# Kernel tuning notes

Hardware: AMD Instinct MI355X
Metric: run time of the kernel (lower is better)

Reference implementation:

```python
import jax, jax.numpy as jnp
import numpy as np

TOPK, NUM_CLASSES = 13, 80
ALPHA, BETA, GAMMA, EPS = 1.0, 5.0, 3.0, 1e-09


def _make_boxes(key, shape, img=640.0, wmin=10.0, wmax=120.0):
    k1, k2 = jax.random.split(key)
    cxy = jax.random.uniform(k1, shape[:-1] + (2,), minval=0.0, maxval=img)
    wh = jax.random.uniform(k2, shape[:-1] + (2,), minval=wmin, maxval=wmax)
    return jnp.concatenate([cxy - wh / 2, cxy + wh / 2], axis=-1)


def setup_inputs() -> dict:
    key = jax.random.key(0)
    ks = jax.random.split(key, 7)
    bs, A, C, n = 16, 8400, 80, 60
    return {
        'pd_scores': jax.random.uniform(ks[0], (bs, A, C), dtype=jnp.float32),
        'pd_bboxes': _make_boxes(ks[1], (bs, A, 4)),
        'pd_angles': jax.random.uniform(ks[2], (bs, A, 1), minval=0.0, maxval=90.0),
        'anc_points': jax.random.uniform(ks[3], (A, 2), minval=0.0, maxval=640.0),
        'gt_labels': jax.random.randint(ks[4], (bs, n, 1), 0, C, dtype=jnp.int32),
        'gt_bboxes': _make_boxes(ks[5], (bs, n, 4)),
        'gt_angles': jax.random.uniform(ks[6], (bs, n, 1), minval=0.0, maxval=90.0),
        'mask_gt': jnp.ones((bs, n, 1), jnp.float32),
        'epoch_num': 1,
    }


def _cos_fn(x, ar, beta=2.0):
    return 0.5 + 0.5 * jnp.cos(beta / ar * x / 180.0 * jnp.pi + jnp.pi * (1.0 - beta / (2.0 * ar)))


def _angle_measure(pd_angles, gt_angles, gt_bboxes):
    # gt area ratio w/h -> (bs, n, 1, 1)
    w = gt_bboxes[..., 2:3] - gt_bboxes[..., 0:1]
    h = gt_bboxes[..., 3:4] - gt_bboxes[..., 1:2]
    ar = (w / (h + 1e-05))[:, :, None, :]
    theta = jnp.abs(gt_angles[:, :, None, :] - pd_angles[:, None, :, :])  # (bs,n,A,1)
    av = 1.0 / ar / (2.0 - 1.0 / ar)
    mx = _cos_fn(0.0, ar)
    mn = _cos_fn(90.0, ar)
    r = (_cos_fn(theta, ar) - mn) / (mx - mn) * (1.0 - av) + av
    r = jnp.where(jnp.isnan(r), 0.0, r)
    return jnp.squeeze(r, -1)  # (bs, n, A)


def _pairwise_iou(gt, pd):
    # gt (bs,n,4), pd (bs,A,4) -> (bs,n,A)
    lt = jnp.maximum(gt[:, :, None, :2], pd[:, None, :, :2])
    rb = jnp.minimum(gt[:, :, None, 2:], pd[:, None, :, 2:])
    inter = jnp.clip(rb - lt, 0.0).prod(-1)
    a1 = jnp.clip(gt[..., 2:] - gt[..., :2], 0.0).prod(-1)[:, :, None]
    a2 = jnp.clip(pd[..., 2:] - pd[..., :2], 0.0).prod(-1)[:, None, :]
    return inter / (a1 + a2 - inter + EPS)


def _select_topk(metrics, topk_mask):
    bs, n, A = metrics.shape
    _, idxs = jax.lax.top_k(metrics, TOPK)
    idxs = jnp.where(topk_mask, idxs, 0)
    flat = idxs.reshape(bs * n, TOPK)
    cnt = jnp.zeros((bs * n, A), jnp.int32).at[jnp.arange(bs * n)[:, None], flat].add(1)
    cnt = cnt.reshape(bs, n, A)
    return jnp.where(cnt > 1, 0, cnt).astype(metrics.dtype)


def _select_highest_overlaps(mask_pos, overlaps, n):
    fg = mask_pos.sum(-2)                                   # (bs, A)
    multi = fg[:, None, :] > 1                              # (bs, 1, A)
    is_max = jax.nn.one_hot(overlaps.argmax(1), n, axis=1, dtype=mask_pos.dtype)  # (bs,n,A)
    mask_pos = jnp.where(multi, is_max, mask_pos)
    fg = mask_pos.sum(-2)
    tgt_idx = mask_pos.argmax(-2)                           # (bs, A)
    return tgt_idx, fg, mask_pos


def reference(pd_scores, pd_bboxes, pd_angles, anc_points, gt_labels, gt_bboxes, gt_angles, mask_gt, epoch_num):
    bs, A, C = pd_scores.shape
    n = gt_bboxes.shape[1]
    lab = gt_labels[..., 0].astype(jnp.int32)               # (bs, n)

    # bbox_scores: pd_scores[b, :, gt_label] -> (bs, n, A)
    pts = jnp.transpose(pd_scores, (0, 2, 1))               # (bs, C, A)
    bbox_scores = jnp.take_along_axis(pts, lab[:, :, None], axis=1)

    overlaps = _pairwise_iou(gt_bboxes, pd_bboxes)          # (bs, n, A)
    ang = _angle_measure(pd_angles, gt_angles, gt_bboxes)   # (bs, n, A)
    align = bbox_scores ** ALPHA * overlaps ** BETA * ang ** GAMMA

    # anchors-inside-gt mask (bs, n, A)
    lt = anc_points[None, None, :, :] - gt_bboxes[:, :, None, :2]
    rb = gt_bboxes[:, :, None, 2:] - anc_points[None, None, :, :]
    in_gts = (jnp.concatenate([lt, rb], -1).min(-1) > EPS).astype(align.dtype)

    topk_mask = jnp.broadcast_to(mask_gt > 0, (bs, n, TOPK))
    mask_topk = _select_topk(align * in_gts, topk_mask)
    mask_pos = mask_topk * in_gts * mask_gt                 # (bs, n, A)

    tgt_idx, fg, mask_pos = _select_highest_overlaps(mask_pos, overlaps, n)

    # gather per-anchor targets from flattened gt tensors
    off = tgt_idx + jnp.arange(bs, dtype=tgt_idx.dtype)[:, None] * n   # (bs, A)
    tlab = lab.reshape(-1)[off]
    tlab = jnp.where(tlab < 0, 0, tlab)
    tbb = gt_bboxes.reshape(-1, 4)[off]                     # (bs, A, 4)
    tang = gt_angles.reshape(-1, 1)[off]                    # (bs, A, 1)
    ts = jax.nn.one_hot(tlab, C, dtype=pd_scores.dtype)     # (bs, A, C)
    ts = jnp.where(fg[:, :, None] > 0, ts, 0.0)

    # normalized alignment metric scaling
    align = align * mask_pos
    pam = align.max(-1, keepdims=True)                      # (bs, n, 1)
    pov = (overlaps * mask_pos).max(-1, keepdims=True)      # (bs, n, 1)
    norm = (align * pov / (pam + EPS)).max(-2)[:, :, None]  # (bs, A, 1)
    ts = ts * norm

    return tlab, tbb, tang, ts, fg > 0
```

## Files before the change

kernel.cpp:

```cpp
#include <hip/hip_runtime.h>
#include <math.h>

#define TOPK 13
#define PI_F 3.14159265358979323846f
#define K1_WAVES 4

typedef unsigned int u32;
typedef unsigned long long u64;

__device__ __forceinline__ u32 ford(float f) {
    u32 u = __float_as_uint(f);
    return (u & 0x80000000u) ? ~u : (u | 0x80000000u);
}
__device__ __forceinline__ float funord(u32 o) {
    u32 u = (o & 0x80000000u) ? (o & 0x7FFFFFFFu) : ~o;
    return __uint_as_float(u);
}

__device__ __forceinline__ float iou_fn(float4 g, float4 p) {
    float ltx = fmaxf(g.x, p.x), lty = fmaxf(g.y, p.y);
    float rbx = fminf(g.z, p.z), rby = fminf(g.w, p.w);
    float inter = fmaxf(rbx - ltx, 0.0f) * fmaxf(rby - lty, 0.0f);
    float a1 = fmaxf(g.z - g.x, 0.0f) * fmaxf(g.w - g.y, 0.0f);
    float a2 = fmaxf(p.z - p.x, 0.0f) * fmaxf(p.w - p.y, 0.0f);
    return inter / (((a1 + a2) - inter) + 1e-9f);
}

struct RowParams { float av, bar, offc, mx, mn; };

__device__ __forceinline__ RowParams row_params(float4 g) {
    float w = g.z - g.x, h = g.w - g.y;
    float ar = w / (h + 1e-5f);
    float ia = 1.0f / ar;
    RowParams rp;
    rp.av = ia / (2.0f - ia);
    rp.bar = 2.0f / ar;
    rp.offc = PI_F * (1.0f - 2.0f / (2.0f * ar));
    rp.mx = 0.5f + 0.5f * cosf(rp.offc);
    rp.mn = 0.5f + 0.5f * cosf(rp.bar * 90.0f / 180.0f * PI_F + rp.offc);
    return rp;
}

__device__ __forceinline__ float ang_measure(const RowParams& rp, float theta) {
    float cfv = 0.5f + 0.5f * cosf(rp.bar * theta / 180.0f * PI_F + rp.offc);
    float r = (cfv - rp.mn) / (rp.mx - rp.mn) * (1.0f - rp.av) + rp.av;
    return isnan(r) ? 0.0f : r;
}

__device__ __forceinline__ float align_fn(float s, float iou, float r) {
    float iou2 = iou * iou;
    float iou5 = (iou2 * iou2) * iou;
    float r3 = (r * r) * r;
    return (s * iou5) * r3;
}

__device__ __forceinline__ void insert13(u64* arr, u64 key) {
    if (key > arr[TOPK - 1]) {
#pragma unroll
        for (int jj = 0; jj < TOPK; jj++) {
            u64 hi = arr[jj] > key ? arr[jj] : key;
            u64 lo = arr[jj] > key ? key : arr[jj];
            arr[jj] = hi;
            key = lo;
        }
    }
}

__global__ void k0_init(int* cnt, int* assign1, u32* pam, u32* pov, int BA, int BN) {
    int t = blockIdx.x * blockDim.x + threadIdx.x;
    if (t < BA) { cnt[t] = 0; assign1[t] = -1; }
    if (t < BN) { pam[t] = 0x80000000u; pov[t] = 0x80000000u; }
}

__global__ __launch_bounds__(256)
void k1_topk(const float* __restrict__ scores, const float* __restrict__ pbox,
             const float* __restrict__ pang, const float* __restrict__ anc,
             const int* __restrict__ glab, const float* __restrict__ gbox,
             const float* __restrict__ gang, const float* __restrict__ mgt,
             int* __restrict__ cnt, int* __restrict__ assign1,
             float* __restrict__ out,
             int bs, int A, int n, int C) {
    int j = blockIdx.x;
    int b = j % bs;
    int i = j / bs;
    int bi = b * n + i;
    int tid = threadIdx.x;
    int BA = bs * A;

    int nF4 = BA * (C / 4);
    int zCH = (nF4 + gridDim.x - 1) / gridDim.x;
    int zBeg = j * zCH + tid;
    int zEnd = min(j * zCH + zCH, nF4);
    float4* tsf4 = (float4*)(out + (size_t)BA * 6);
    const float4 z4 = make_float4(0.0f, 0.0f, 0.0f, 0.0f);

    float mg = mgt[bi];
    if (!(mg > 0.0f)) {
        for (; zBeg < zEnd; zBeg += 256) tsf4[zBeg] = z4;
        return;
    }

    float4 g = ((const float4*)gbox)[bi];
    int lab = glab[bi];
    float ga = gang[bi];
    RowParams rp = row_params(g);

    const float4* pb = ((const float4*)pbox) + (size_t)b * A;
    const float* pa = pang + (size_t)b * A;
    const float2* ac = (const float2*)anc;
    const float* sc = scores + (size_t)b * A * C + lab;

    u64 arr[TOPK];
#pragma unroll
    for (int jj = 0; jj < TOPK; jj++) arr[jj] = 0ull;
    u64 zkey = 0ull;

    int a = tid;
    float4 p = pb[a];
    float pav = pa[a];
    float2 apt = ac[a];
    float mnv = fminf(fminf(apt.x - g.x, apt.y - g.y), fminf(g.z - apt.x, g.w - apt.y));

    int nit = (A + 255) >> 8;
    int clampA = A - 1;
    for (int it = 0; it < nit; ++it) {
        int an = a + 256;
        int can = min(an, clampA);
        float4 p2 = pb[can];
        float pav2 = pa[can];
        float2 apt2 = ac[can];
        if (zBeg < zEnd) { tsf4[zBeg] = z4; zBeg += 256; }
        float mnv2 = fminf(fminf(apt2.x - g.x, apt2.y - g.y),
                           fminf(g.z - apt2.x, g.w - apt2.y));

        bool valid = a < A;
        float iou = iou_fn(g, p);
        bool needAlign = (mnv > 1e-9f) && (iou > 0.0f) && valid;
        if (needAlign || (zkey == 0ull && valid)) {
            float th = fabsf(ga - pav);
            float r = ang_measure(rp, th);
            bool zeroCand;
            if (needAlign && r > 0.0f) {
                float s = sc[(size_t)a * C];
                float v = align_fn(s, iou, r);
                if (v > 0.0f) {
                    zeroCand = false;
                    insert13(arr, ((u64)ford(v) << 32) | (u64)(0xFFFFFFFFu - (u32)a));
                } else {
                    zeroCand = true;
                }
            } else {
                zeroCand = (r >= 0.0f);
            }
            if (zeroCand && zkey == 0ull) {
                zkey = (0x80000000ull << 32) | (u64)(0xFFFFFFFFu - (u32)a);
            }
        }
        a = an; p = p2; pav = pav2; mnv = mnv2;
    }
    for (; zBeg < zEnd; zBeg += 256) tsf4[zBeg] = z4;
    insert13(arr, zkey);

    __shared__ u64 wtop[K1_WAVES * TOPK];
    int lane = tid & 63, wv = tid >> 6;
    for (int round = 0; round < TOPK; round++) {
        u64 m = arr[0];
#pragma unroll
        for (int st = 32; st > 0; st >>= 1) {
            u64 o = __shfl_xor(m, st, 64);
            if (o > m) m = o;
        }
        if (lane == 0) wtop[wv * TOPK + round] = m;
        if (arr[0] == m && m != 0ull) {
#pragma unroll
            for (int jj = 0; jj < TOPK - 1; jj++) arr[jj] = arr[jj + 1];
            arr[TOPK - 1] = 0ull;
        }
    }
    __syncthreads();

    if (wv == 0) {
        const int NK = K1_WAVES * TOPK;
        u64 ka = (lane < NK) ? wtop[lane] : 0ull;
        for (int round = 0; round < TOPK; round++) {
            u64 m = ka;
#pragma unroll
            for (int st = 32; st > 0; st >>= 1) {
                u64 o = __shfl_xor(m, st, 64);
                if (o > m) m = o;
            }
            if (m == 0ull) break;
            if (ka == m) {
                ka = 0ull;
                int aa = (int)(0xFFFFFFFFu - (u32)(m & 0xFFFFFFFFull));
                float2 ap2 = ac[aa];
                float mnw = fminf(fminf(ap2.x - g.x, ap2.y - g.y),
                                  fminf(g.z - ap2.x, g.w - ap2.y));
                if (mnw > 1e-9f) {
                    atomicAdd(&cnt[(size_t)b * A + aa], 1);
                    atomicMax(&assign1[(size_t)b * A + aa], i);
                }
            }
        }
    }
}

__global__ __launch_bounds__(256)
void k2_resolve(const float* __restrict__ scores, const float* __restrict__ pbox,
                const float* __restrict__ pang, const int* __restrict__ glab,
                const float* __restrict__ gbox, const float* __restrict__ gang,
                const int* __restrict__ cnt, const int* __restrict__ assign1,
                int* __restrict__ assign, float* __restrict__ alignv,
                u32* __restrict__ pam, u32* __restrict__ pov,
                int bs, int A, int n, int C) {
    int t = blockIdx.x * blockDim.x + threadIdx.x;
    if (t >= bs * A) return;
    int b = t / A;
    int c = cnt[t];
    int asg = -1;
    float alv = 0.0f;
    if (c > 0) {
        float4 p = ((const float4*)pbox)[t];
        if (c == 1) {
            asg = assign1[t];
        } else {
            float best = -1.0f;
            asg = 0;
            for (int i = 0; i < n; i++) {
                float4 gi = ((const float4*)gbox)[b * n + i];
                float io = iou_fn(gi, p);
                if (io > best) { best = io; asg = i; }
            }
        }
        float4 g = ((const float4*)gbox)[b * n + asg];
        RowParams rp = row_params(g);
        float iou = iou_fn(g, p);
        float th = fabsf(gang[b * n + asg] - pang[t]);
        float r = ang_measure(rp, th);
        float s = scores[(size_t)t * C + glab[b * n + asg]];
        alv = align_fn(s, iou, r);
        atomicMax(&pam[b * n + asg], ford(alv));
        atomicMax(&pov[b * n + asg], ford(iou));
    }
    assign[t] = asg;
    alignv[t] = alv;
}

__global__ __launch_bounds__(256)
void k3_out(const int* __restrict__ glab, const float* __restrict__ gbox,
            const float* __restrict__ gang, const int* __restrict__ assign,
            const float* __restrict__ alignv, const u32* __restrict__ pam,
            const u32* __restrict__ pov, float* __restrict__ out,
            int bs, int A, int n, int C) {
    int t = blockIdx.x * blockDim.x + threadIdx.x;
    int BA = bs * A;
    if (t >= BA) return;
    int b = t / A;
    int asg = assign[t];
    bool fg = asg >= 0;
    int tgt = fg ? asg : 0;
    int lb = glab[b * n + tgt];
    if (lb < 0) lb = 0;

    out[t] = (float)lb;
    ((float4*)(out + BA))[t] = ((const float4*)gbox)[b * n + tgt];
    out[(size_t)BA * 5 + t] = gang[b * n + tgt];
    out[(size_t)BA * 6 + (size_t)BA * C + t] = fg ? 1.0f : 0.0f;

    if (fg) {
        float pamv = funord(pam[b * n + asg]);
        float povv = funord(pov[b * n + asg]);
        float vv = (alignv[t] * povv) / (pamv + 1e-9f);
        out[(size_t)BA * 6 + (size_t)t * C + lb] = fmaxf(vv, 0.0f);
    }
}

extern "C" void kernel_launch(void* const* d_in, const int* in_sizes, int n_in,
                              void* d_out, int out_size, void* d_ws, size_t ws_size,
                              hipStream_t stream) {
    const float* scores = (const float*)d_in[0];
    const float* pbox = (const float*)d_in[1];
    const float* pang = (const float*)d_in[2];
    const float* anc = (const float*)d_in[3];
    const int* glab = (const int*)d_in[4];
    const float* gbox = (const float*)d_in[5];
    const float* gang = (const float*)d_in[6];
    const float* mgt = (const float*)d_in[7];

    const int C = 80;
    int A = in_sizes[3] / 2;
    int bs = in_sizes[0] / (A * C);
    int n = in_sizes[4] / bs;
    int BA = bs * A;
    int BN = bs * n;

    char* ws = (char*)d_ws;
    int* cnt = (int*)ws;        ws += sizeof(int) * (size_t)BA;
    int* assign1 = (int*)ws;    ws += sizeof(int) * (size_t)BA;
    int* assign = (int*)ws;     ws += sizeof(int) * (size_t)BA;
    float* alignv = (float*)ws; ws += sizeof(float) * (size_t)BA;
    u32* pam = (u32*)ws;        ws += sizeof(u32) * (size_t)BN;
    u32* pov = (u32*)ws;        ws += sizeof(u32) * (size_t)BN;

    k0_init<<<(BA + 255) / 256, 256, 0, stream>>>(cnt, assign1, pam, pov, BA, BN);
    k1_topk<<<BN, 256, 0, stream>>>(scores, pbox, pang, anc, glab, gbox, gang, mgt,
                                    cnt, assign1, (float*)d_out, bs, A, n, C);
    k2_resolve<<<(BA + 255) / 256, 256, 0, stream>>>(scores, pbox, pang, glab, gbox, gang,
                                                     cnt, assign1, assign, alignv, pam, pov,
                                                     bs, A, n, C);
    k3_out<<<(BA + 255) / 256, 256, 0, stream>>>(glab, gbox, gang, assign, alignv, pam, pov,
                                                 (float*)d_out, bs, A, n, C);
}
```

Before: 161.5 us.

## Stage per-anchor inputs through double-buffered LDS with async global-to-LDS loads

Replaces the register-level one-iteration prefetch of predicted boxes, angles and anchor points with chunked asynchronous global_load_lds copies into double-buffered shared memory. Different waves load different arrays for the next chunk while the current chunk is processed from LDS. The intent is to hide global latency and reduce register pressure. In exchange it adds a block-wide barrier per chunk and relies on correct completion ordering for the async loads.

```diff
diff --git a/kernel.cpp b/kernel.cpp
--- a/kernel.cpp
+++ b/kernel.cpp
@@ -4,9 +4,13 @@
 #define TOPK 13
 #define PI_F 3.14159265358979323846f
 #define K1_WAVES 4
+#define CHK 256
 
 typedef unsigned int u32;
 typedef unsigned long long u64;
+
+typedef const __attribute__((address_space(1))) void* gas_t;
+typedef __attribute__((address_space(3))) void* las_t;
 
 __device__ __forceinline__ u32 ford(float f) {
     u32 u = __float_as_uint(f);
@@ -110,59 +114,81 @@
     const float2* ac = (const float2*)anc;
     const float* sc = scores + (size_t)b * A * C + lab;
 
+    __shared__ __align__(16) float4 bufP[2][CHK];
+    __shared__ __align__(16) float  bufQ[2][CHK];
+    __shared__ __align__(16) float2 bufC[2][CHK];
+
+    int lane = tid & 63, wv = tid >> 6;
+    int nch = (A + CHK - 1) / CHK;
+
+    auto stage = [&](int c, int bufIdx) {
+        int gi = min(c * CHK + wv * 64 + lane, A - 1);
+        __builtin_amdgcn_global_load_lds((gas_t)(const void*)&pb[gi],
+                                         (las_t)(void*)&bufP[bufIdx][wv * 64],
+                                         16, 0, 0);
+        if (wv == 0) {
+            int qs = min(c * CHK + lane * 4, A - 4);
+            __builtin_amdgcn_global_load_lds((gas_t)(const void*)&pa[qs],
+                                             (las_t)(void*)&bufQ[bufIdx][0],
+                                             16, 0, 0);
+        } else if (wv <= 2) {
+            int k = wv - 1;
+            int cs = min(c * CHK + k * 128 + lane * 2, A - 2);
+            __builtin_amdgcn_global_load_lds((gas_t)(const void*)&ac[cs],
+                                             (las_t)(void*)&bufC[bufIdx][k * 128],
+                                             16, 0, 0);
+        }
+    };
+
     u64 arr[TOPK];
 #pragma unroll
     for (int jj = 0; jj < TOPK; jj++) arr[jj] = 0ull;
     u64 zkey = 0ull;
 
-    int a = tid;
-    float4 p = pb[a];
-    float pav = pa[a];
-    float2 apt = ac[a];
-    float mnv = fminf(fminf(apt.x - g.x, apt.y - g.y), fminf(g.z - apt.x, g.w - apt.y));
-
-    int nit = (A + 255) >> 8;
-    int clampA = A - 1;
-    for (int it = 0; it < nit; ++it) {
-        int an = a + 256;
-        int can = min(an, clampA);
-        float4 p2 = pb[can];
-        float pav2 = pa[can];
-        float2 apt2 = ac[can];
+    stage(0, 0);
+    __syncthreads();
+
+    for (int c = 0; c < nch; ++c) {
+        int cb = c & 1;
+        if (c + 1 < nch) stage(c + 1, cb ^ 1);
         if (zBeg < zEnd) { tsf4[zBeg] = z4; zBeg += 256; }
-        float mnv2 = fminf(fminf(apt2.x - g.x, apt2.y - g.y),
-                           fminf(g.z - apt2.x, g.w - apt2.y));
-
-        bool valid = a < A;
-        float iou = iou_fn(g, p);
-        bool needAlign = (mnv > 1e-9f) && (iou > 0.0f) && valid;
-        if (needAlign || (zkey == 0ull && valid)) {
-            float th = fabsf(ga - pav);
-            float r = ang_measure(rp, th);
-            bool zeroCand;
-            if (needAlign && r > 0.0f) {
-                float s = sc[(size_t)a * C];
-                float v = align_fn(s, iou, r);
-                if (v > 0.0f) {
-                    zeroCand = false;
-                    insert13(arr, ((u64)ford(v) << 32) | (u64)(0xFFFFFFFFu - (u32)a));
+
+        int a = c * CHK + tid;
+        if (a < A) {
+            float4 p = bufP[cb][tid];
+            float pav = bufQ[cb][tid];
+            float2 apt = bufC[cb][tid];
+            float iou = iou_fn(g, p);
+            float mnv = fminf(fminf(apt.x - g.x, apt.y - g.y),
+                              fminf(g.z - apt.x, g.w - apt.y));
+            bool needAlign = (mnv > 1e-9f) && (iou > 0.0f);
+            if (needAlign || zkey == 0ull) {
+                float th = fabsf(ga - pav);
+                float r = ang_measure(rp, th);
+                bool zeroCand;
+                if (needAlign && r > 0.0f) {
+                    float s = sc[(size_t)a * C];
+                    float v = align_fn(s, iou, r);
+                    if (v > 0.0f) {
+                        zeroCand = false;
+                        insert13(arr, ((u64)ford(v) << 32) | (u64)(0xFFFFFFFFu - (u32)a));
+                    } else {
+                        zeroCand = true;
+                    }
                 } else {
-                    zeroCand = true;
+                    zeroCand = (r >= 0.0f);
                 }
-            } else {
-                zeroCand = (r >= 0.0f);
+                if (zeroCand && zkey == 0ull) {
+                    zkey = (0x80000000ull << 32) | (u64)(0xFFFFFFFFu - (u32)a);
+                }
             }
-            if (zeroCand && zkey == 0ull) {
-                zkey = (0x80000000ull << 32) | (u64)(0xFFFFFFFFu - (u32)a);
-            }
-        }
-        a = an; p = p2; pav = pav2; mnv = mnv2;
+        }
+        __syncthreads();
     }
     for (; zBeg < zEnd; zBeg += 256) tsf4[zBeg] = z4;
     insert13(arr, zkey);
 
     __shared__ u64 wtop[K1_WAVES * TOPK];
-    int lane = tid & 63, wv = tid >> 6;
     for (int round = 0; round < TOPK; round++) {
         u64 m = arr[0];
 #pragma unroll
```

After: 170.8 us. +5.8%, slower.

## Process four GT rows per block with shared-memory candidate lists

Applied to the files above, without the earlier changes.

The top-k kernel now handles four ground-truth rows per block, so each pass over the predicted boxes, angles and anchors serves four rows instead of one. The per-thread 13-entry register insertion sort is replaced by appending positive candidates to a 64-entry shared list via shared atomics, plus a per-thread zero-candidate key. Each wave then merges one row by repeated wave-max rounds. If a row has more than 64 positives it falls back to a slow rescan of all anchors, one pass per top-k round. This cuts the grid to a quarter and removes redundant global reads and register pressure, at the cost of more per-thread work and the overflow risk. Because the zeroing loop now advances twice per iteration while the block count drops, the output-zeroing chunk per block looks different.

```diff
diff --git a/kernel.cpp b/kernel.cpp
--- a/kernel.cpp
+++ b/kernel.cpp
@@ -3,7 +3,8 @@
 
 #define TOPK 13
 #define PI_F 3.14159265358979323846f
-#define K1_WAVES 4
+#define RPB 4
+#define CAP 64
 
 typedef unsigned int u32;
 typedef unsigned long long u64;
@@ -54,18 +55,6 @@
     return (s * iou5) * r3;
 }
 
-__device__ __forceinline__ void insert13(u64* arr, u64 key) {
-    if (key > arr[TOPK - 1]) {
-#pragma unroll
-        for (int jj = 0; jj < TOPK; jj++) {
-            u64 hi = arr[jj] > key ? arr[jj] : key;
-            u64 lo = arr[jj] > key ? key : arr[jj];
-            arr[jj] = hi;
-            key = lo;
-        }
-    }
-}
-
 __global__ void k0_init(int* cnt, int* assign1, u32* pam, u32* pov, int BA, int BN) {
     int t = blockIdx.x * blockDim.x + threadIdx.x;
     if (t < BA) { cnt[t] = 0; assign1[t] = -1; }
@@ -82,8 +71,8 @@
              int bs, int A, int n, int C) {
     int j = blockIdx.x;
     int b = j % bs;
-    int i = j / bs;
-    int bi = b * n + i;
+    int rg = j / bs;
+    int i0 = rg * RPB;
     int tid = threadIdx.x;
     int BA = bs * A;
 
@@ -94,32 +83,56 @@
     float4* tsf4 = (float4*)(out + (size_t)BA * 6);
     const float4 z4 = make_float4(0.0f, 0.0f, 0.0f, 0.0f);
 
-    float mg = mgt[bi];
-    if (!(mg > 0.0f)) {
-        for (; zBeg < zEnd; zBeg += 256) tsf4[zBeg] = z4;
-        return;
-    }
-
-    float4 g = ((const float4*)gbox)[bi];
-    int lab = glab[bi];
-    float ga = gang[bi];
-    RowParams rp = row_params(g);
+    __shared__ u64 posL[RPB][CAP];
+    __shared__ u64 zdump[RPB][256];
+    __shared__ int pc[RPB];
+    __shared__ int ovfrows[RPB];
+    __shared__ int novf;
+    __shared__ u64 red[4];
+
+    if (tid < RPB) pc[tid] = 0;
+    if (tid == 0) novf = 0;
+
+    float4 g[RPB];
+    float rpav[RPB], rpbar[RPB], rpoff[RPB], rpmx[RPB], rpmn[RPB];
+    float ga[RPB];
+    int lab[RPB];
+    bool act[RPB];
+#pragma unroll
+    for (int r = 0; r < RPB; ++r) {
+        int i = i0 + r;
+        act[r] = false;
+        g[r] = make_float4(0.0f, 0.0f, 0.0f, 0.0f);
+        ga[r] = 0.0f; lab[r] = 0;
+        rpav[r] = rpbar[r] = rpoff[r] = rpmx[r] = rpmn[r] = 0.0f;
+        if (i < n) {
+            int bi = b * n + i;
+            if (mgt[bi] > 0.0f) {
+                act[r] = true;
+                g[r] = ((const float4*)gbox)[bi];
+                RowParams rp = row_params(g[r]);
+                rpav[r] = rp.av; rpbar[r] = rp.bar; rpoff[r] = rp.offc;
+                rpmx[r] = rp.mx; rpmn[r] = rp.mn;
+                ga[r] = gang[bi];
+                lab[r] = glab[bi];
+            }
+        }
+    }
+    __syncthreads();
 
     const float4* pb = ((const float4*)pbox) + (size_t)b * A;
     const float* pa = pang + (size_t)b * A;
     const float2* ac = (const float2*)anc;
-    const float* sc = scores + (size_t)b * A * C + lab;
-
-    u64 arr[TOPK];
+    const float* scb = scores + (size_t)b * A * C;
+
+    u64 zkey[RPB];
 #pragma unroll
-    for (int jj = 0; jj < TOPK; jj++) arr[jj] = 0ull;
-    u64 zkey = 0ull;
+    for (int r = 0; r < RPB; ++r) zkey[r] = 0ull;
 
     int a = tid;
     float4 p = pb[a];
     float pav = pa[a];
     float2 apt = ac[a];
-    float mnv = fminf(fminf(apt.x - g.x, apt.y - g.y), fminf(g.z - apt.x, g.w - apt.y));
 
     int nit = (A + 255) >> 8;
     int clampA = A - 1;
@@ -130,77 +143,156 @@
         float pav2 = pa[can];
         float2 apt2 = ac[can];
         if (zBeg < zEnd) { tsf4[zBeg] = z4; zBeg += 256; }
-        float mnv2 = fminf(fminf(apt2.x - g.x, apt2.y - g.y),
-                           fminf(g.z - apt2.x, g.w - apt2.y));
-
-        bool valid = a < A;
-        float iou = iou_fn(g, p);
-        bool needAlign = (mnv > 1e-9f) && (iou > 0.0f) && valid;
-        if (needAlign || (zkey == 0ull && valid)) {
-            float th = fabsf(ga - pav);
-            float r = ang_measure(rp, th);
-            bool zeroCand;
-            if (needAlign && r > 0.0f) {
-                float s = sc[(size_t)a * C];
-                float v = align_fn(s, iou, r);
-                if (v > 0.0f) {
-                    zeroCand = false;
-                    insert13(arr, ((u64)ford(v) << 32) | (u64)(0xFFFFFFFFu - (u32)a));
-                } else {
-                    zeroCand = true;
+        if (zBeg < zEnd) { tsf4[zBeg] = z4; zBeg += 256; }
+        if (a < A) {
+#pragma unroll
+            for (int r = 0; r < RPB; ++r) {
+                if (!act[r]) continue;
+                float mnv = fminf(fminf(apt.x - g[r].x, apt.y - g[r].y),
+                                  fminf(g[r].z - apt.x, g[r].w - apt.y));
+                float iou = iou_fn(g[r], p);
+                bool na = (mnv > 1e-9f) && (iou > 0.0f);
+                if (na || zkey[r] == 0ull) {
+                    RowParams rp;
+                    rp.av = rpav[r]; rp.bar = rpbar[r]; rp.offc = rpoff[r];
+                    rp.mx = rpmx[r]; rp.mn = rpmn[r];
+                    float th = fabsf(ga[r] - pav);
+                    float rr = ang_measure(rp, th);
+                    bool zc;
+                    if (na && rr > 0.0f) {
+                        float s = scb[(size_t)a * C + lab[r]];
+                        float v = align_fn(s, iou, rr);
+                        if (v > 0.0f) {
+                            zc = false;
+                            u64 key = ((u64)ford(v) << 32) | (u64)(0xFFFFFFFFu - (u32)a);
+                            int idx = atomicAdd(&pc[r], 1);
+                            if (idx < CAP) posL[r][idx] = key;
+                        } else zc = true;
+                    } else zc = (rr >= 0.0f);
+                    if (zc && zkey[r] == 0ull)
+                        zkey[r] = (0x80000000ull << 32) | (u64)(0xFFFFFFFFu - (u32)a);
                 }
-            } else {
-                zeroCand = (r >= 0.0f);
-            }
-            if (zeroCand && zkey == 0ull) {
-                zkey = (0x80000000ull << 32) | (u64)(0xFFFFFFFFu - (u32)a);
             }
         }
-        a = an; p = p2; pav = pav2; mnv = mnv2;
+        a = an; p = p2; pav = pav2; apt = apt2;
     }
     for (; zBeg < zEnd; zBeg += 256) tsf4[zBeg] = z4;
-    insert13(arr, zkey);
-
-    __shared__ u64 wtop[K1_WAVES * TOPK];
+
+#pragma unroll
+    for (int r = 0; r < RPB; ++r) zdump[r][tid] = zkey[r];
+    __syncthreads();
+
     int lane = tid & 63, wv = tid >> 6;
-    for (int round = 0; round < TOPK; round++) {
-        u64 m = arr[0];
-#pragma unroll
-        for (int st = 32; st > 0; st >>= 1) {
-            u64 o = __shfl_xor(m, st, 64);
-            if (o > m) m = o;
-        }
-        if (lane == 0) wtop[wv * TOPK + round] = m;
-        if (arr[0] == m && m != 0ull) {
-#pragma unroll
-            for (int jj = 0; jj < TOPK - 1; jj++) arr[jj] = arr[jj + 1];
-            arr[TOPK - 1] = 0ull;
-        }
-    }
+
+#define MERGE_ROW(RR)                                                          \
+    {                                                                          \
+        if (act[RR]) {                                                         \
+            int P = pc[RR];                                                    \
+            if (P <= CAP) {                                                    \
+                u64 s0 = (lane < P) ? posL[RR][lane] : 0ull;                   \
+                u64 s1 = zdump[RR][lane];                                      \
+                u64 s2 = zdump[RR][lane + 64];                                 \
+                u64 s3 = zdump[RR][lane + 128];                                \
+                u64 s4 = zdump[RR][lane + 192];                                \
+                for (int round = 0; round < TOPK; ++round) {                   \
+                    u64 m = s0;                                                \
+                    if (s1 > m) m = s1;                                        \
+                    if (s2 > m) m = s2;                                        \
+                    if (s3 > m) m = s3;                                        \
+                    if (s4 > m) m = s4;                                        \
+                    for (int st = 32; st > 0; st >>= 1) {                      \
+                        u64 o = __shfl_xor(m, st, 64);                         \
+                        if (o > m) m = o;                                      \
+                    }                                                          \
+                    if (m == 0ull) break;                                      \
+                    bool own = false;                                          \
+                    if (s0 == m) { s0 = 0ull; own = true; }                    \
+                    else if (s1 == m) { s1 = 0ull; own = true; }               \
+                    else if (s2 == m) { s2 = 0ull; own = true; }               \
+                    else if (s3 == m) { s3 = 0ull; own = true; }               \
+                    else if (s4 == m) { s4 = 0ull; own = true; }               \
+                    if (own) {                                                 \
+                        int aa = (int)(0xFFFFFFFFu - (u32)(m & 0xFFFFFFFFull));\
+                        float2 ap2 = ac[aa];                                   \
+                        float mnw = fminf(fminf(ap2.x - g[RR].x,               \
+                                                ap2.y - g[RR].y),              \
+                                          fminf(g[RR].z - ap2.x,               \
+                                                g[RR].w - ap2.y));             \
+                        if (mnw > 1e-9f) {                                     \
+                            atomicAdd(&cnt[(size_t)b * A + aa], 1);            \
+                            atomicMax(&assign1[(size_t)b * A + aa], i0 + RR);  \
+                        }                                                      \
+                    }                                                          \
+                }                                                              \
+            } else if (lane == 0) {                                            \
+                int o = atomicAdd(&novf, 1);                                   \
+                ovfrows[o] = RR;                                               \
+            }                                                                  \
+        }                                                                      \
+    }
+
+    if (wv == 0) MERGE_ROW(0)
+    else if (wv == 1) MERGE_ROW(1)
+    else if (wv == 2) MERGE_ROW(2)
+    else MERGE_ROW(3)
+#undef MERGE_ROW
     __syncthreads();
 
-    if (wv == 0) {
-        const int NK = K1_WAVES * TOPK;
-        u64 ka = (lane < NK) ? wtop[lane] : 0ull;
-        for (int round = 0; round < TOPK; round++) {
-            u64 m = ka;
-#pragma unroll
+    for (int k = 0; k < novf; ++k) {
+        int rI = ovfrows[k];
+        int i = i0 + rI;
+        int bi = b * n + i;
+        float4 gg = ((const float4*)gbox)[bi];
+        RowParams rpp = row_params(gg);
+        float gga = gang[bi];
+        int ll = glab[bi];
+        u64 last = 0xFFFFFFFFFFFFFFFFull;
+        for (int round = 0; round < TOPK; ++round) {
+            u64 best = 0ull;
+            for (int aa = tid; aa < A; aa += 256) {
+                float2 ap2 = ac[aa];
+                float4 pp = pb[aa];
+                float mnv = fminf(fminf(ap2.x - gg.x, ap2.y - gg.y),
+                                  fminf(gg.z - ap2.x, gg.w - ap2.y));
+                float iou = iou_fn(gg, pp);
+                bool na = (mnv > 1e-9f) && (iou > 0.0f);
+                float th = fabsf(gga - pa[aa]);
+                float rr = ang_measure(rpp, th);
+                u64 zk = (0x80000000ull << 32) | (u64)(0xFFFFFFFFu - (u32)aa);
+                u64 key = 0ull;
+                if (na && rr > 0.0f) {
+                    float s = scb[(size_t)aa * C + ll];
+                    float v = align_fn(s, iou, rr);
+                    key = (v > 0.0f)
+                        ? (((u64)ford(v) << 32) | (u64)(0xFFFFFFFFu - (u32)aa))
+                        : zk;
+                } else if (rr >= 0.0f) key = zk;
+                if (key < last && key > best) best = key;
+            }
+            u64 m = best;
             for (int st = 32; st > 0; st >>= 1) {
                 u64 o = __shfl_xor(m, st, 64);
                 if (o > m) m = o;
             }
-            if (m == 0ull) break;
-            if (ka == m) {
-                ka = 0ull;
-                int aa = (int)(0xFFFFFFFFu - (u32)(m & 0xFFFFFFFFull));
-                float2 ap2 = ac[aa];
-                float mnw = fminf(fminf(ap2.x - g.x, ap2.y - g.y),
-                                  fminf(g.z - ap2.x, g.w - ap2.y));
+            if (lane == 0) red[wv] = m;
+            __syncthreads();
+            u64 win = red[0];
+            if (red[1] > win) win = red[1];
+            if (red[2] > win) win = red[2];
+            if (red[3] > win) win = red[3];
+            __syncthreads();
+            if (win == 0ull) break;
+            int aw = (int)(0xFFFFFFFFu - (u32)(win & 0xFFFFFFFFull));
+            if ((aw & 255) == tid) {
+                float2 ap2 = ac[aw];
+                float mnw = fminf(fminf(ap2.x - gg.x, ap2.y - gg.y),
+                                  fminf(gg.z - ap2.x, gg.w - ap2.y));
                 if (mnw > 1e-9f) {
-                    atomicAdd(&cnt[(size_t)b * A + aa], 1);
-                    atomicMax(&assign1[(size_t)b * A + aa], i);
+                    atomicAdd(&cnt[(size_t)b * A + aw], 1);
+                    atomicMax(&assign1[(size_t)b * A + aw], i);
                 }
             }
+            last = win;
         }
     }
 }
@@ -302,9 +394,11 @@
     u32* pam = (u32*)ws;        ws += sizeof(u32) * (size_t)BN;
     u32* pov = (u32*)ws;        ws += sizeof(u32) * (size_t)BN;
 
+    int NG = (n + RPB - 1) / RPB;
+
     k0_init<<<(BA + 255) / 256, 256, 0, stream>>>(cnt, assign1, pam, pov, BA, BN);
-    k1_topk<<<BN, 256, 0, stream>>>(scores, pbox, pang, anc, glab, gbox, gang, mgt,
-                                    cnt, assign1, (float*)d_out, bs, A, n, C);
+    k1_topk<<<bs * NG, 256, 0, stream>>>(scores, pbox, pang, anc, glab, gbox, gang, mgt,
+                                         cnt, assign1, (float*)d_out, bs, A, n, C);
     k2_resolve<<<(BA + 255) / 256, 256, 0, stream>>>(scores, pbox, pang, glab, gbox, gang,
                                                      cnt, assign1, assign, alignv, pam, pov,
                                                      bs, A, n, C);
```

Result: slower. 174.9 us (+8.3%).
